# Performance work log

Hardware: AMD Instinct MI355X
Metric: run time of the kernel (lower is better)

## Reference

```python
import jax, jax.numpy as jnp
import numpy as np

HID = 64  # self.hidden_num

def setup_inputs() -> dict:
    key = jax.random.key(0)
    ks = jax.random.split(key, 6)
    B, C_IN, N, T, C_OUT = 2, 64, 128, 24, 64
    x = jax.random.normal(ks[0], (B, C_IN, N, T), dtype=jnp.float32)
    attention = jax.random.uniform(ks[1], (B, 1, N, N, T), dtype=jnp.float32)
    # agg_fc1: Linear(c_in, 64); agg_fc2: Linear(128, c_out). Store weights as [in, out].
    s1 = 1.0 / np.sqrt(C_IN)
    s2 = 1.0 / np.sqrt(2 * HID)
    W1 = jax.random.uniform(ks[2], (C_IN, HID), jnp.float32, -s1, s1)
    b1 = jax.random.uniform(ks[3], (HID,), jnp.float32, -s1, s1)
    W2 = jax.random.uniform(ks[4], (2 * HID, C_OUT), jnp.float32, -s2, s2)
    b2 = jax.random.uniform(ks[5], (C_OUT,), jnp.float32, -s2, s2)
    return {"x": x, "attention": attention, "W1": W1, "b1": b1, "W2": W2, "b2": b2}

def reference(x, attention, W1, b1, W2, b2):
    # x: [B, H, N, T] -> [B, N, T, H]
    xp = jnp.transpose(x, (0, 2, 3, 1))
    h = xp @ W1 + b1  # [B, N, T, HID]
    # Original: concat(v_feature, h_feature) @ W2 where v=h_i (dim 1=dest i), h=h_j (dim 2=src j).
    # Exact decomposition: message[b,i,j,t] = h[b,i,t]@W2v + h[b,j,t]@W2h + b2,
    # avoiding the O(N^2) concat tensor.
    mv = h @ W2[:HID]   # [B, N, T, C_OUT] (dest part)
    mh = h @ W2[HID:]   # [B, N, T, C_OUT] (src part)
    a = attention[:, 0]  # [B, N(i), N(j), T]
    asum = jnp.sum(a, axis=2)  # [B, N, T]
    upd = asum[..., None] * (mv + b2) + jnp.einsum('bijt,bjtc->bitc', a, mh)
    return jnp.transpose(upd, (0, 3, 1, 2))  # [B, C_OUT, N, T]
```

## Files before the change

kernel.cpp:

```cpp
#include <hip/hip_runtime.h>

constexpr int B_   = 2;
constexpr int CIN  = 64;
constexpr int N    = 128;
constexpr int T    = 24;
constexpr int HID  = 64;
constexpr int COUT = 64;
constexpr int NT   = N * T;
constexpr int BT   = B_ * T;
constexpr int ATT_BLOCKS = B_ * N;
constexpr int XT_BLOCKS  = 32;
constexpr int WF_BLOCKS  = 16;
constexpr int PREP_BLOCKS = ATT_BLOCKS + XT_BLOCKS + WF_BLOCKS;

typedef __attribute__((ext_vector_type(8))) short short8;
typedef __attribute__((ext_vector_type(4))) float f32x4;

__device__ inline unsigned short f2bf(float f) {
    unsigned u = __float_as_uint(f);
    return (unsigned short)((u + 0x7FFFu + ((u >> 16) & 1u)) >> 16);
}

__global__ __launch_bounds__(256) void k_prep(
    const float* __restrict__ x,
    const float* __restrict__ att,
    const float* __restrict__ W1,
    const float* __restrict__ b1,
    const float* __restrict__ W2,
    const float* __restrict__ b2,
    unsigned* __restrict__ xT32,
    unsigned* __restrict__ attT32,
    float* __restrict__ asum_g,
    unsigned short* __restrict__ WfvT,
    unsigned short* __restrict__ WfhT,
    float* __restrict__ bvb2,
    float* __restrict__ bh)
{
    __shared__ __align__(16) unsigned smem_u32[8320];
    const int tid = threadIdx.x;
    const int blk = blockIdx.x;

    if (blk < ATT_BLOCKS) {
        float* ts   = (float*)smem_u32;
        float* psum = ts + 3200;
        const int b = blk >> 7;
        const int i = blk & 127;

        const float* ab = att + ((size_t)b * N + i) * NT;
#pragma unroll
        for (int u = 0; u < 12; ++u) {
            const int idx = tid + 256 * u;
            const int j = idx / T, t = idx - j * T;
            ts[j * 25 + t] = ab[idx];
        }
        __syncthreads();
#pragma unroll
        for (int u = 0; u < 6; ++u) {
            const int e2 = tid + 256 * u;
            const int t = e2 >> 6, jp = e2 & 63, j = jp * 2;
            const unsigned pk = (unsigned)f2bf(ts[j * 25 + t])
                              | ((unsigned)f2bf(ts[(j + 1) * 25 + t]) << 16);
            attT32[((size_t)(b * T + t) * N + i) * 64 + jp] = pk;
        }
        if (tid < 192) {
            const int t = tid >> 3, p = tid & 7;
            float s = 0.f;
#pragma unroll
            for (int q = 0; q < 16; ++q) s += ts[(p * 16 + q) * 25 + t];
            psum[t * 8 + p] = s;
        }
        __syncthreads();
        if (tid < T) {
            float s = 0.f;
#pragma unroll
            for (int p = 0; p < 8; ++p) s += psum[tid * 8 + p];
            asum_g[(size_t)(b * T + tid) * N + i] = s;
        }
    } else if (blk < ATT_BLOCKS + XT_BLOCKS) {
        const int tb = blk - ATT_BLOCKS;
        const int b  = tb >> 4;
        const int n0 = (tb & 15) * 8;
#pragma unroll
        for (int u = 0; u < 12; ++u) {
            const int vidx = tid + 256 * u;
            const int cp = vidx / 48, w48 = vidx - cp * 48;
            const float4 v = *(const float4*)(x + (size_t)(b * CIN + cp) * NT
                                              + n0 * T + w48 * 4);
            smem_u32[cp * 97 + w48 * 2]     = (unsigned)f2bf(v.x) | ((unsigned)f2bf(v.y) << 16);
            smem_u32[cp * 97 + w48 * 2 + 1] = (unsigned)f2bf(v.z) | ((unsigned)f2bf(v.w) << 16);
        }
        __syncthreads();
#pragma unroll
        for (int v = 0; v < 24; ++v) {
            const int oidx = tid + 256 * v;
            const int t = oidx >> 8, rem = oidx & 255;
            const int n = rem >> 5, cp = rem & 31;
            const int r = n * T + t;
            const unsigned w0 = smem_u32[(2 * cp) * 97 + (r >> 1)];
            const unsigned w1 = smem_u32[(2 * cp + 1) * 97 + (r >> 1)];
            const unsigned v0 = (r & 1) ? (w0 >> 16) : (w0 & 0xFFFFu);
            const unsigned v1 = (r & 1) ? (w1 >> 16) : (w1 & 0xFFFFu);
            xT32[((size_t)(b * T + t) * N + n0 + n) * 32 + cp] = v0 | (v1 << 16);
        }
    } else {
        const int wf   = blk - (ATT_BLOCKS + XT_BLOCKS);
        const int half = wf >> 3;
        const int c0   = (wf & 7) * 8;
        float* sW1 = (float*)smem_u32;
        float* sW2 = sW1 + 64 * 65;
#pragma unroll
        for (int u = 0; u < 16; ++u) {
            const int i = tid + 256 * u;
            const int r = i >> 6, q = i & 63;
            sW1[r * 65 + q] = W1[i];
            sW2[r * 65 + q] = W2[half * 4096 + i];
        }
        __syncthreads();

        const int c = c0 + (tid & 7);
        const int r = tid >> 3;
        float a0 = 0.f, a1 = 0.f;
#pragma unroll
        for (int q = 0; q < 64; ++q) {
            const float w2 = sW2[q * 65 + c];
            a0 += sW1[r * 65 + q] * w2;
            a1 += sW1[(r + 32) * 65 + q] * w2;
        }
        unsigned short* dst = half ? WfhT : WfvT;
        dst[c * 64 + r]      = f2bf(a0);
        dst[c * 64 + r + 32] = f2bf(a1);

        if (tid < 8) {
            const int cb = c0 + tid;
            float s = 0.f;
#pragma unroll
            for (int q = 0; q < 64; ++q) s += b1[q] * sW2[q * 65 + cb];
            if (half) bh[cb] = s;
            else      bvb2[cb] = s + b2[cb];
        }
    }
}

__global__ __launch_bounds__(256) void k_all(
    const unsigned short* __restrict__ xTb,
    const unsigned short* __restrict__ attTb,
    const unsigned short* __restrict__ WfvT,
    const unsigned short* __restrict__ WfhT,
    const float* __restrict__ bvb2,
    const float* __restrict__ bh,
    const float* __restrict__ asum_g,
    float* __restrict__ out)
{
    __shared__ __align__(8) unsigned short mhT[64][140];

    const int blk   = blockIdx.x;
    const int itile = blk & 7;
    const int bt    = blk >> 3;
    const int b     = bt / T;
    const int t     = bt - b * T;

    const int tid  = threadIdx.x;
    const int w    = tid >> 6;
    const int lane = tid & 63;
    const int c16  = lane & 15;
    const int q4   = lane >> 4;
    const int cc   = w * 16 + c16;

    const unsigned short* whr = WfhT + cc * 64;
    const short8 wh0 = *(const short8*)(whr + q4 * 8);
    const short8 wh1 = *(const short8*)(whr + 32 + q4 * 8);
    const unsigned short* wvr = WfvT + cc * 64;
    const short8 wv0 = *(const short8*)(wvr + q4 * 8);
    const short8 wv1 = *(const short8*)(wvr + 32 + q4 * 8);
    const float bhc = bh[cc];
    const float bvc = bvb2[cc];

    const unsigned short* xpanel = xTb + (size_t)bt * N * CIN;

    f32x4 accv = {0.f, 0.f, 0.f, 0.f};
#pragma unroll
    for (int nt8 = 0; nt8 < 8; ++nt8) {
        const unsigned short* xr = xpanel + (nt8 * 16 + c16) * CIN;
        const short8 a0 = *(const short8*)(xr + q4 * 8);
        const short8 a1 = *(const short8*)(xr + 32 + q4 * 8);
        f32x4 d = {0.f, 0.f, 0.f, 0.f};
        d = __builtin_amdgcn_mfma_f32_16x16x32_bf16(a0, wh0, d, 0, 0, 0);
        d = __builtin_amdgcn_mfma_f32_16x16x32_bf16(a1, wh1, d, 0, 0, 0);
        uint2 pk;
        pk.x = (unsigned)f2bf(d[0] + bhc) | ((unsigned)f2bf(d[1] + bhc) << 16);
        pk.y = (unsigned)f2bf(d[2] + bhc) | ((unsigned)f2bf(d[3] + bhc) << 16);
        *(uint2*)&mhT[cc][nt8 * 16 + q4 * 4] = pk;
        if (nt8 == itile) {
            accv = __builtin_amdgcn_mfma_f32_16x16x32_bf16(a0, wv0, accv, 0, 0, 0);
            accv = __builtin_amdgcn_mfma_f32_16x16x32_bf16(a1, wv1, accv, 0, 0, 0);
        }
    }
    __syncthreads();

    f32x4 acc = {0.f, 0.f, 0.f, 0.f};
    const unsigned short* arow = attTb + ((size_t)bt * N + itile * 16 + c16) * N;
#pragma unroll
    for (int ks = 0; ks < 4; ++ks) {
        const short8 a  = *(const short8*)(arow + ks * 32 + q4 * 8);
        const short8 bb = *(const short8*)(&mhT[cc][ks * 32 + q4 * 8]);
        acc = __builtin_amdgcn_mfma_f32_16x16x32_bf16(a, bb, acc, 0, 0, 0);
    }

    const int il0 = itile * 16 + q4 * 4;
    const f32x4 as4 = *(const f32x4*)(asum_g + (size_t)bt * N + il0);
    float* ob = out + (((size_t)b * COUT + cc) * N + il0) * T + t;
#pragma unroll
    for (int e = 0; e < 4; ++e) {
        ob[e * T] = acc[e] + as4[e] * (accv[e] + bvc);
    }
}

extern "C" void kernel_launch(void* const* d_in, const int* in_sizes, int n_in,
                              void* d_out, int out_size, void* d_ws, size_t ws_size,
                              hipStream_t stream)
{
    const float* x   = (const float*)d_in[0];
    const float* att = (const float*)d_in[1];
    const float* W1  = (const float*)d_in[2];
    const float* b1  = (const float*)d_in[3];
    const float* W2  = (const float*)d_in[4];
    const float* b2  = (const float*)d_in[5];
    float* out = (float*)d_out;

    char* ws = (char*)d_ws;
    unsigned*       xT32   = (unsigned*)ws;
    unsigned*       attT32 = (unsigned*)(ws + 786432);
    float*          asum_g = (float*)(ws + 2359296);
    unsigned short* WfvT   = (unsigned short*)(ws + 2383872);
    unsigned short* WfhT   = (unsigned short*)(ws + 2392064);
    float*          bvb2   = (float*)(ws + 2400256);
    float*          bh     = (float*)(ws + 2400512);

    k_prep<<<PREP_BLOCKS, 256, 0, stream>>>(x, att, W1, b1, W2, b2,
                                            xT32, attT32, asum_g,
                                            WfvT, WfhT, bvb2, bh);
    k_all<<<BT * 8, 256, 0, stream>>>((const unsigned short*)xT32,
                                      (const unsigned short*)attT32,
                                      WfvT, WfhT, bvb2, bh, asum_g, out);
}
```

Measured before the change: 18.69 us.

## Split main kernel into single-wave blocks and add transpose kernel for output

The fused kernel now runs one wavefront per block over a 16-channel tile, so it launches four times as many blocks and needs no block barrier. The attention loads are hoisted ahead of the projection MFMAs. Results go to a workspace in [bt, n, c] order, and a new third kernel transposes them through shared memory into the [B, C, N, T] output with coalesced writes. This removes the strided scattered stores and the __syncthreads, but each block now recomputes the mh projection for every channel tile and the change adds a kernel launch plus an extra round trip through global memory.

```diff
diff --git a/kernel.cpp b/kernel.cpp
--- a/kernel.cpp
+++ b/kernel.cpp
@@ -12,6 +12,7 @@
 constexpr int XT_BLOCKS  = 32;
 constexpr int WF_BLOCKS  = 16;
 constexpr int PREP_BLOCKS = ATT_BLOCKS + XT_BLOCKS + WF_BLOCKS;
+constexpr int ALL_BLOCKS  = BT * 8 * 4;
 
 typedef __attribute__((ext_vector_type(8))) short short8;
 typedef __attribute__((ext_vector_type(4))) float f32x4;
@@ -141,7 +142,7 @@
     }
 }
 
-__global__ __launch_bounds__(256) void k_all(
+__global__ __launch_bounds__(64) void k_all(
     const unsigned short* __restrict__ xTb,
     const unsigned short* __restrict__ attTb,
     const unsigned short* __restrict__ WfvT,
@@ -149,22 +150,28 @@
     const float* __restrict__ bvb2,
     const float* __restrict__ bh,
     const float* __restrict__ asum_g,
-    float* __restrict__ out)
-{
-    __shared__ __align__(8) unsigned short mhT[64][140];
+    float* __restrict__ upd)
+{
+    __shared__ __align__(8) unsigned short mhT[16][140];
 
     const int blk   = blockIdx.x;
-    const int itile = blk & 7;
-    const int bt    = blk >> 3;
-    const int b     = bt / T;
-    const int t     = bt - b * T;
-
-    const int tid  = threadIdx.x;
-    const int w    = tid >> 6;
-    const int lane = tid & 63;
+    const int ct    = blk & 3;
+    const int itile = (blk >> 2) & 7;
+    const int bt    = blk >> 5;
+
+    const int lane = threadIdx.x & 63;
     const int c16  = lane & 15;
     const int q4   = lane >> 4;
-    const int cc   = w * 16 + c16;
+    const int cc   = ct * 16 + c16;
+
+    const unsigned short* arow = attTb + ((size_t)bt * N + itile * 16 + c16) * N;
+    const short8 at0 = *(const short8*)(arow + 0 * 32 + q4 * 8);
+    const short8 at1 = *(const short8*)(arow + 1 * 32 + q4 * 8);
+    const short8 at2 = *(const short8*)(arow + 2 * 32 + q4 * 8);
+    const short8 at3 = *(const short8*)(arow + 3 * 32 + q4 * 8);
+
+    const int il0 = itile * 16 + q4 * 4;
+    const f32x4 as4 = *(const f32x4*)(asum_g + (size_t)bt * N + il0);
 
     const unsigned short* whr = WfhT + cc * 64;
     const short8 wh0 = *(const short8*)(whr + q4 * 8);
@@ -189,29 +196,50 @@
         uint2 pk;
         pk.x = (unsigned)f2bf(d[0] + bhc) | ((unsigned)f2bf(d[1] + bhc) << 16);
         pk.y = (unsigned)f2bf(d[2] + bhc) | ((unsigned)f2bf(d[3] + bhc) << 16);
-        *(uint2*)&mhT[cc][nt8 * 16 + q4 * 4] = pk;
+        *(uint2*)&mhT[c16][nt8 * 16 + q4 * 4] = pk;
         if (nt8 == itile) {
             accv = __builtin_amdgcn_mfma_f32_16x16x32_bf16(a0, wv0, accv, 0, 0, 0);
             accv = __builtin_amdgcn_mfma_f32_16x16x32_bf16(a1, wv1, accv, 0, 0, 0);
         }
     }
+
+    f32x4 acc = {0.f, 0.f, 0.f, 0.f};
+    acc = __builtin_amdgcn_mfma_f32_16x16x32_bf16(at0, *(const short8*)(&mhT[c16][0 * 32 + q4 * 8]), acc, 0, 0, 0);
+    acc = __builtin_amdgcn_mfma_f32_16x16x32_bf16(at1, *(const short8*)(&mhT[c16][1 * 32 + q4 * 8]), acc, 0, 0, 0);
+    acc = __builtin_amdgcn_mfma_f32_16x16x32_bf16(at2, *(const short8*)(&mhT[c16][2 * 32 + q4 * 8]), acc, 0, 0, 0);
+    acc = __builtin_amdgcn_mfma_f32_16x16x32_bf16(at3, *(const short8*)(&mhT[c16][3 * 32 + q4 * 8]), acc, 0, 0, 0);
+
+    float* ub = upd + ((size_t)bt * N + il0) * COUT + cc;
+#pragma unroll
+    for (int e = 0; e < 4; ++e) {
+        ub[e * COUT] = acc[e] + as4[e] * (accv[e] + bvc);
+    }
+}
+
+__global__ __launch_bounds__(256) void k_out(
+    const float* __restrict__ upd,
+    float* __restrict__ out)
+{
+    __shared__ float ts[T][COUT + 1];
+
+    const int tid = threadIdx.x;
+    const int b   = blockIdx.x >> 7;
+    const int i   = blockIdx.x & 127;
+
+#pragma unroll
+    for (int u = 0; u < 6; ++u) {
+        const int idx = tid + 256 * u;
+        const int t   = idx >> 6;
+        const int c   = idx & 63;
+        ts[t][c] = upd[((size_t)(b * T + t) * N + i) * COUT + c];
+    }
     __syncthreads();
-
-    f32x4 acc = {0.f, 0.f, 0.f, 0.f};
-    const unsigned short* arow = attTb + ((size_t)bt * N + itile * 16 + c16) * N;
-#pragma unroll
-    for (int ks = 0; ks < 4; ++ks) {
-        const short8 a  = *(const short8*)(arow + ks * 32 + q4 * 8);
-        const short8 bb = *(const short8*)(&mhT[cc][ks * 32 + q4 * 8]);
-        acc = __builtin_amdgcn_mfma_f32_16x16x32_bf16(a, bb, acc, 0, 0, 0);
-    }
-
-    const int il0 = itile * 16 + q4 * 4;
-    const f32x4 as4 = *(const f32x4*)(asum_g + (size_t)bt * N + il0);
-    float* ob = out + (((size_t)b * COUT + cc) * N + il0) * T + t;
-#pragma unroll
-    for (int e = 0; e < 4; ++e) {
-        ob[e * T] = acc[e] + as4[e] * (accv[e] + bvc);
+#pragma unroll
+    for (int u = 0; u < 6; ++u) {
+        const int idx = tid + 256 * u;
+        const int c   = idx / T;
+        const int t   = idx - c * T;
+        out[((size_t)(b * COUT + c) * N + i) * T + t] = ts[t][c];
     }
 }
 
@@ -235,11 +263,13 @@
     unsigned short* WfhT   = (unsigned short*)(ws + 2392064);
     float*          bvb2   = (float*)(ws + 2400256);
     float*          bh     = (float*)(ws + 2400512);
+    float*          upd    = (float*)(ws + 2400768);
 
     k_prep<<<PREP_BLOCKS, 256, 0, stream>>>(x, att, W1, b1, W2, b2,
                                             xT32, attT32, asum_g,
                                             WfvT, WfhT, bvb2, bh);
-    k_all<<<BT * 8, 256, 0, stream>>>((const unsigned short*)xT32,
-                                      (const unsigned short*)attT32,
-                                      WfvT, WfhT, bvb2, bh, asum_g, out);
-}
+    k_all<<<ALL_BLOCKS, 64, 0, stream>>>((const unsigned short*)xT32,
+                                         (const unsigned short*)attT32,
+                                         WfvT, WfhT, bvb2, bh, asum_g, upd);
+    k_out<<<B_ * N, 256, 0, stream>>>(upd, out);
+}
```

New measurement: 19.44 us. 1.04x slower.

## Split fused kernel into mh/mv projection kernel and attention aggregation kernel

Applied to the files above, without the earlier changes.

Before, each of the 8 i-tile blocks per (b,t) recomputed the full mh projection for all 128 nodes in shared memory. Now a middle kernel computes mh (bf16) and mv+bias (fp32) once per (b,t) and writes them to workspace. A final kernel reads them for the attention MFMA and the epilogue. This removes the 8x redundant projection work but adds an extra kernel launch and a global round trip for the intermediates.

```diff
diff --git a/kernel.cpp b/kernel.cpp
--- a/kernel.cpp
+++ b/kernel.cpp
@@ -12,6 +12,8 @@
 constexpr int XT_BLOCKS  = 32;
 constexpr int WF_BLOCKS  = 16;
 constexpr int PREP_BLOCKS = ATT_BLOCKS + XT_BLOCKS + WF_BLOCKS;
+constexpr int MID_BLOCKS  = BT * 4;
+constexpr int FIN_BLOCKS  = BT * 8;
 
 typedef __attribute__((ext_vector_type(8))) short short8;
 typedef __attribute__((ext_vector_type(4))) float f32x4;
@@ -141,23 +143,19 @@
     }
 }
 
-__global__ __launch_bounds__(256) void k_all(
+__global__ __launch_bounds__(256) void k_mid(
     const unsigned short* __restrict__ xTb,
-    const unsigned short* __restrict__ attTb,
     const unsigned short* __restrict__ WfvT,
     const unsigned short* __restrict__ WfhT,
     const float* __restrict__ bvb2,
     const float* __restrict__ bh,
-    const float* __restrict__ asum_g,
-    float* __restrict__ out)
-{
-    __shared__ __align__(8) unsigned short mhT[64][140];
-
-    const int blk   = blockIdx.x;
-    const int itile = blk & 7;
-    const int bt    = blk >> 3;
-    const int b     = bt / T;
-    const int t     = bt - b * T;
+    unsigned short* __restrict__ mhT,
+    float* __restrict__ mvT)
+{
+    const int blk  = blockIdx.x;
+    const int nt32 = blk & 3;
+    const int bt   = blk >> 2;
+    const int n0   = nt32 * 32;
 
     const int tid  = threadIdx.x;
     const int w    = tid >> 6;
@@ -177,41 +175,74 @@
 
     const unsigned short* xpanel = xTb + (size_t)bt * N * CIN;
 
-    f32x4 accv = {0.f, 0.f, 0.f, 0.f};
-#pragma unroll
-    for (int nt8 = 0; nt8 < 8; ++nt8) {
-        const unsigned short* xr = xpanel + (nt8 * 16 + c16) * CIN;
+#pragma unroll
+    for (int rt = 0; rt < 2; ++rt) {
+        const int nbase = n0 + rt * 16;
+        const unsigned short* xr = xpanel + (nbase + c16) * CIN;
         const short8 a0 = *(const short8*)(xr + q4 * 8);
         const short8 a1 = *(const short8*)(xr + 32 + q4 * 8);
-        f32x4 d = {0.f, 0.f, 0.f, 0.f};
-        d = __builtin_amdgcn_mfma_f32_16x16x32_bf16(a0, wh0, d, 0, 0, 0);
-        d = __builtin_amdgcn_mfma_f32_16x16x32_bf16(a1, wh1, d, 0, 0, 0);
+
+        f32x4 dh = {0.f, 0.f, 0.f, 0.f};
+        dh = __builtin_amdgcn_mfma_f32_16x16x32_bf16(a0, wh0, dh, 0, 0, 0);
+        dh = __builtin_amdgcn_mfma_f32_16x16x32_bf16(a1, wh1, dh, 0, 0, 0);
+        f32x4 dv = {0.f, 0.f, 0.f, 0.f};
+        dv = __builtin_amdgcn_mfma_f32_16x16x32_bf16(a0, wv0, dv, 0, 0, 0);
+        dv = __builtin_amdgcn_mfma_f32_16x16x32_bf16(a1, wv1, dv, 0, 0, 0);
+
+        const int nn = nbase + q4 * 4;
         uint2 pk;
-        pk.x = (unsigned)f2bf(d[0] + bhc) | ((unsigned)f2bf(d[1] + bhc) << 16);
-        pk.y = (unsigned)f2bf(d[2] + bhc) | ((unsigned)f2bf(d[3] + bhc) << 16);
-        *(uint2*)&mhT[cc][nt8 * 16 + q4 * 4] = pk;
-        if (nt8 == itile) {
-            accv = __builtin_amdgcn_mfma_f32_16x16x32_bf16(a0, wv0, accv, 0, 0, 0);
-            accv = __builtin_amdgcn_mfma_f32_16x16x32_bf16(a1, wv1, accv, 0, 0, 0);
-        }
-    }
-    __syncthreads();
+        pk.x = (unsigned)f2bf(dh[0] + bhc) | ((unsigned)f2bf(dh[1] + bhc) << 16);
+        pk.y = (unsigned)f2bf(dh[2] + bhc) | ((unsigned)f2bf(dh[3] + bhc) << 16);
+        *(uint2*)&mhT[((size_t)bt * COUT + cc) * N + nn] = pk;
+
+        f32x4 v;
+        v[0] = dv[0] + bvc; v[1] = dv[1] + bvc;
+        v[2] = dv[2] + bvc; v[3] = dv[3] + bvc;
+        *(f32x4*)&mvT[((size_t)bt * COUT + cc) * N + nn] = v;
+    }
+}
+
+__global__ __launch_bounds__(256) void k_fin(
+    const unsigned short* __restrict__ attTb,
+    const unsigned short* __restrict__ mhT,
+    const float* __restrict__ mvT,
+    const float* __restrict__ asum_g,
+    float* __restrict__ out)
+{
+    const int blk   = blockIdx.x;
+    const int itile = blk & 7;
+    const int bt    = blk >> 3;
+    const int b     = bt / T;
+    const int t     = bt - b * T;
+
+    const int tid  = threadIdx.x;
+    const int w    = tid >> 6;
+    const int lane = tid & 63;
+    const int c16  = lane & 15;
+    const int q4   = lane >> 4;
+    const int n0   = w * 16;
+
+    const unsigned short* arow = attTb + ((size_t)bt * N + itile * 16 + c16) * N;
+    const unsigned short* brow = mhT   + ((size_t)bt * COUT + n0 + c16) * N;
 
     f32x4 acc = {0.f, 0.f, 0.f, 0.f};
-    const unsigned short* arow = attTb + ((size_t)bt * N + itile * 16 + c16) * N;
 #pragma unroll
     for (int ks = 0; ks < 4; ++ks) {
         const short8 a  = *(const short8*)(arow + ks * 32 + q4 * 8);
-        const short8 bb = *(const short8*)(&mhT[cc][ks * 32 + q4 * 8]);
+        const short8 bb = *(const short8*)(brow + ks * 32 + q4 * 8);
         acc = __builtin_amdgcn_mfma_f32_16x16x32_bf16(a, bb, acc, 0, 0, 0);
     }
 
     const int il0 = itile * 16 + q4 * 4;
+    const int cc  = n0 + c16;
+
+    const f32x4 mb  = *(const f32x4*)(mvT + ((size_t)bt * COUT + cc) * N + il0);
     const f32x4 as4 = *(const f32x4*)(asum_g + (size_t)bt * N + il0);
+
     float* ob = out + (((size_t)b * COUT + cc) * N + il0) * T + t;
 #pragma unroll
     for (int e = 0; e < 4; ++e) {
-        ob[e * T] = acc[e] + as4[e] * (accv[e] + bvc);
+        ob[e * T] = acc[e] + as4[e] * mb[e];
     }
 }
 
@@ -235,11 +266,14 @@
     unsigned short* WfhT   = (unsigned short*)(ws + 2392064);
     float*          bvb2   = (float*)(ws + 2400256);
     float*          bh     = (float*)(ws + 2400512);
+    unsigned short* mhT    = (unsigned short*)(ws + 2400768);
+    float*          mvT    = (float*)(ws + 3187200);
 
     k_prep<<<PREP_BLOCKS, 256, 0, stream>>>(x, att, W1, b1, W2, b2,
                                             xT32, attT32, asum_g,
                                             WfvT, WfhT, bvb2, bh);
-    k_all<<<BT * 8, 256, 0, stream>>>((const unsigned short*)xT32,
-                                      (const unsigned short*)attT32,
-                                      WfvT, WfhT, bvb2, bh, asum_g, out);
-}
+    k_mid<<<MID_BLOCKS, 256, 0, stream>>>((const unsigned short*)xT32,
+                                          WfvT, WfhT, bvb2, bh, mhT, mvT);
+    k_fin<<<FIN_BLOCKS, 256, 0, stream>>>((const unsigned short*)attT32,
+                                          mhT, mvT, asum_g, out);
+}
```

New measurement: 19.52 us. +4.5%, slower.

## Repartition main kernel by channel half to remove redundant mh recomputation

Applied to the files above, without the earlier changes.

Before, each of the 8 i-tile blocks per (b,t) recomputed the full mh projection for all 128 nodes. Now each (b,t) is split into two blocks by output-channel half, with 512 threads (8 waves), and each wave computes mh and mv for its own 16 nodes once. The results are shared through LDS, and the attention tile is prefetched before the projection. This removes redundant projection MFMAs and x reloads, but the grid shrinks from 384 to 96 blocks, which lowers parallelism across CUs.

```diff
diff --git a/kernel.cpp b/kernel.cpp
--- a/kernel.cpp
+++ b/kernel.cpp
@@ -12,6 +12,7 @@
 constexpr int XT_BLOCKS  = 32;
 constexpr int WF_BLOCKS  = 16;
 constexpr int PREP_BLOCKS = ATT_BLOCKS + XT_BLOCKS + WF_BLOCKS;
+constexpr int MAIN_BLOCKS = BT * 2;
 
 typedef __attribute__((ext_vector_type(8))) short short8;
 typedef __attribute__((ext_vector_type(4))) float f32x4;
@@ -141,7 +142,7 @@
     }
 }
 
-__global__ __launch_bounds__(256) void k_all(
+__global__ __launch_bounds__(512) void k_main(
     const unsigned short* __restrict__ xTb,
     const unsigned short* __restrict__ attTb,
     const unsigned short* __restrict__ WfvT,
@@ -151,67 +152,92 @@
     const float* __restrict__ asum_g,
     float* __restrict__ out)
 {
-    __shared__ __align__(8) unsigned short mhT[64][140];
+    __shared__ __align__(8) unsigned short mh_lds[32][136];
+    __shared__ __align__(16) float         mv_lds[32][132];
 
     const int blk   = blockIdx.x;
-    const int itile = blk & 7;
-    const int bt    = blk >> 3;
+    const int chalf = blk & 1;
+    const int bt    = blk >> 1;
     const int b     = bt / T;
     const int t     = bt - b * T;
+    const int c0    = chalf * 32;
 
     const int tid  = threadIdx.x;
     const int w    = tid >> 6;
     const int lane = tid & 63;
     const int c16  = lane & 15;
     const int q4   = lane >> 4;
-    const int cc   = w * 16 + c16;
-
-    const unsigned short* whr = WfhT + cc * 64;
-    const short8 wh0 = *(const short8*)(whr + q4 * 8);
-    const short8 wh1 = *(const short8*)(whr + 32 + q4 * 8);
-    const unsigned short* wvr = WfvT + cc * 64;
-    const short8 wv0 = *(const short8*)(wvr + q4 * 8);
-    const short8 wv1 = *(const short8*)(wvr + 32 + q4 * 8);
-    const float bhc = bh[cc];
-    const float bvc = bvb2[cc];
-
-    const unsigned short* xpanel = xTb + (size_t)bt * N * CIN;
-
-    f32x4 accv = {0.f, 0.f, 0.f, 0.f};
-#pragma unroll
-    for (int nt8 = 0; nt8 < 8; ++nt8) {
-        const unsigned short* xr = xpanel + (nt8 * 16 + c16) * CIN;
-        const short8 a0 = *(const short8*)(xr + q4 * 8);
-        const short8 a1 = *(const short8*)(xr + 32 + q4 * 8);
-        f32x4 d = {0.f, 0.f, 0.f, 0.f};
-        d = __builtin_amdgcn_mfma_f32_16x16x32_bf16(a0, wh0, d, 0, 0, 0);
-        d = __builtin_amdgcn_mfma_f32_16x16x32_bf16(a1, wh1, d, 0, 0, 0);
-        uint2 pk;
-        pk.x = (unsigned)f2bf(d[0] + bhc) | ((unsigned)f2bf(d[1] + bhc) << 16);
-        pk.y = (unsigned)f2bf(d[2] + bhc) | ((unsigned)f2bf(d[3] + bhc) << 16);
-        *(uint2*)&mhT[cc][nt8 * 16 + q4 * 4] = pk;
-        if (nt8 == itile) {
-            accv = __builtin_amdgcn_mfma_f32_16x16x32_bf16(a0, wv0, accv, 0, 0, 0);
-            accv = __builtin_amdgcn_mfma_f32_16x16x32_bf16(a1, wv1, accv, 0, 0, 0);
+
+    const unsigned short* arow = attTb + ((size_t)bt * N + w * 16 + c16) * N;
+    const short8 at0 = *(const short8*)(arow + 0 * 32 + q4 * 8);
+    const short8 at1 = *(const short8*)(arow + 1 * 32 + q4 * 8);
+    const short8 at2 = *(const short8*)(arow + 2 * 32 + q4 * 8);
+    const short8 at3 = *(const short8*)(arow + 3 * 32 + q4 * 8);
+    const int il0 = w * 16 + q4 * 4;
+    const f32x4 as4 = *(const f32x4*)(asum_g + (size_t)bt * N + il0);
+
+    const int cc0 = c0 + c16;
+    const int cc1 = c0 + 16 + c16;
+    const short8 wh00 = *(const short8*)(WfhT + cc0 * 64 + q4 * 8);
+    const short8 wh01 = *(const short8*)(WfhT + cc0 * 64 + 32 + q4 * 8);
+    const short8 wh10 = *(const short8*)(WfhT + cc1 * 64 + q4 * 8);
+    const short8 wh11 = *(const short8*)(WfhT + cc1 * 64 + 32 + q4 * 8);
+    const short8 wv00 = *(const short8*)(WfvT + cc0 * 64 + q4 * 8);
+    const short8 wv01 = *(const short8*)(WfvT + cc0 * 64 + 32 + q4 * 8);
+    const short8 wv10 = *(const short8*)(WfvT + cc1 * 64 + q4 * 8);
+    const short8 wv11 = *(const short8*)(WfvT + cc1 * 64 + 32 + q4 * 8);
+    const float bh0 = bh[cc0],   bh1 = bh[cc1];
+    const float bv0 = bvb2[cc0], bv1 = bvb2[cc1];
+
+    const unsigned short* xr = xTb + ((size_t)bt * N + w * 16 + c16) * CIN;
+    const short8 a0 = *(const short8*)(xr + q4 * 8);
+    const short8 a1 = *(const short8*)(xr + 32 + q4 * 8);
+
+    f32x4 dh0 = {0.f,0.f,0.f,0.f}, dh1 = {0.f,0.f,0.f,0.f};
+    f32x4 dv0 = {0.f,0.f,0.f,0.f}, dv1 = {0.f,0.f,0.f,0.f};
+    dh0 = __builtin_amdgcn_mfma_f32_16x16x32_bf16(a0, wh00, dh0, 0, 0, 0);
+    dh0 = __builtin_amdgcn_mfma_f32_16x16x32_bf16(a1, wh01, dh0, 0, 0, 0);
+    dh1 = __builtin_amdgcn_mfma_f32_16x16x32_bf16(a0, wh10, dh1, 0, 0, 0);
+    dh1 = __builtin_amdgcn_mfma_f32_16x16x32_bf16(a1, wh11, dh1, 0, 0, 0);
+    dv0 = __builtin_amdgcn_mfma_f32_16x16x32_bf16(a0, wv00, dv0, 0, 0, 0);
+    dv0 = __builtin_amdgcn_mfma_f32_16x16x32_bf16(a1, wv01, dv0, 0, 0, 0);
+    dv1 = __builtin_amdgcn_mfma_f32_16x16x32_bf16(a0, wv10, dv1, 0, 0, 0);
+    dv1 = __builtin_amdgcn_mfma_f32_16x16x32_bf16(a1, wv11, dv1, 0, 0, 0);
+
+    {
+        const int nn = w * 16 + q4 * 4;
+        uint2 p0;
+        p0.x = (unsigned)f2bf(dh0[0] + bh0) | ((unsigned)f2bf(dh0[1] + bh0) << 16);
+        p0.y = (unsigned)f2bf(dh0[2] + bh0) | ((unsigned)f2bf(dh0[3] + bh0) << 16);
+        *(uint2*)&mh_lds[c16][nn] = p0;
+        uint2 p1;
+        p1.x = (unsigned)f2bf(dh1[0] + bh1) | ((unsigned)f2bf(dh1[1] + bh1) << 16);
+        p1.y = (unsigned)f2bf(dh1[2] + bh1) | ((unsigned)f2bf(dh1[3] + bh1) << 16);
+        *(uint2*)&mh_lds[16 + c16][nn] = p1;
+#pragma unroll
+        for (int e = 0; e < 4; ++e) {
+            mv_lds[c16][nn + e]      = dv0[e] + bv0;
+            mv_lds[16 + c16][nn + e] = dv1[e] + bv1;
         }
     }
     __syncthreads();
 
-    f32x4 acc = {0.f, 0.f, 0.f, 0.f};
-    const unsigned short* arow = attTb + ((size_t)bt * N + itile * 16 + c16) * N;
+    f32x4 acc0 = {0.f,0.f,0.f,0.f}, acc1 = {0.f,0.f,0.f,0.f};
 #pragma unroll
     for (int ks = 0; ks < 4; ++ks) {
-        const short8 a  = *(const short8*)(arow + ks * 32 + q4 * 8);
-        const short8 bb = *(const short8*)(&mhT[cc][ks * 32 + q4 * 8]);
-        acc = __builtin_amdgcn_mfma_f32_16x16x32_bf16(a, bb, acc, 0, 0, 0);
-    }
-
-    const int il0 = itile * 16 + q4 * 4;
-    const f32x4 as4 = *(const f32x4*)(asum_g + (size_t)bt * N + il0);
-    float* ob = out + (((size_t)b * COUT + cc) * N + il0) * T + t;
+        const short8 a = (ks == 0) ? at0 : (ks == 1) ? at1 : (ks == 2) ? at2 : at3;
+        const short8 b0 = *(const short8*)(&mh_lds[c16][ks * 32 + q4 * 8]);
+        const short8 b1v = *(const short8*)(&mh_lds[16 + c16][ks * 32 + q4 * 8]);
+        acc0 = __builtin_amdgcn_mfma_f32_16x16x32_bf16(a, b0,  acc0, 0, 0, 0);
+        acc1 = __builtin_amdgcn_mfma_f32_16x16x32_bf16(a, b1v, acc1, 0, 0, 0);
+    }
+
+    float* ob0 = out + (((size_t)b * COUT + cc0) * N + il0) * T + t;
+    float* ob1 = out + (((size_t)b * COUT + cc1) * N + il0) * T + t;
 #pragma unroll
     for (int e = 0; e < 4; ++e) {
-        ob[e * T] = acc[e] + as4[e] * (accv[e] + bvc);
+        ob0[e * T] = acc0[e] + as4[e] * mv_lds[c16][il0 + e];
+        ob1[e * T] = acc1[e] + as4[e] * mv_lds[16 + c16][il0 + e];
     }
 }
 
@@ -239,7 +265,7 @@
     k_prep<<<PREP_BLOCKS, 256, 0, stream>>>(x, att, W1, b1, W2, b2,
                                             xT32, attT32, asum_g,
                                             WfvT, WfhT, bvb2, bh);
-    k_all<<<BT * 8, 256, 0, stream>>>((const unsigned short*)xT32,
-                                      (const unsigned short*)attT32,
-                                      WfvT, WfhT, bvb2, bh, asum_g, out);
-}
+    k_main<<<MAIN_BLOCKS, 512, 0, stream>>>((const unsigned short*)xT32,
+                                            (const unsigned short*)attT32,
+                                            WfvT, WfhT, bvb2, bh, asum_g, out);
+}
```

Result: no change. 18.38 us (-1.6%).
